# Optimization experiments

Hardware: AMD Instinct MI355X
Metric: run time of the kernel (lower is better)

## Reference

```python
import jax, jax.numpy as jnp
import numpy as np

DIM = 1024
HEADS = 16
HEAD_DIM = DIM // HEADS
EPS = 1e-6

def _layernorm(x, gamma, beta):
    # LayerNorm over last axis (head_dim), biased variance like torch
    mu = jnp.mean(x, axis=-1, keepdims=True)
    var = jnp.mean(jnp.square(x - mu), axis=-1, keepdims=True)
    return (x - mu) * jax.lax.rsqrt(var + EPS) * gamma + beta

def setup_inputs() -> dict:
    key = jax.random.key(0)
    ks = jax.random.split(key, 12)
    B, N, D = 2, 2048, DIM
    s = 1.0 / np.sqrt(D)
    inp = {
        'x': jax.random.normal(ks[0], (B, N, D), jnp.float32),
        'attn_bias': jax.random.normal(ks[1], (B, 1, N, N), jnp.float32),
        'Wq': jax.random.normal(ks[2], (D, D), jnp.float32) * s,
        'bq': jnp.zeros((D,), jnp.float32),
        'Wk': jax.random.normal(ks[3], (D, D), jnp.float32) * s,
        'bk': jnp.zeros((D,), jnp.float32),
        'Wv': jax.random.normal(ks[4], (D, D), jnp.float32) * s,
        'bv': jnp.zeros((D,), jnp.float32),
        'Wo': jax.random.normal(ks[5], (D, D), jnp.float32) * s,
        'bo': jnp.zeros((D,), jnp.float32),
        'q_gamma': jnp.ones((HEAD_DIM,), jnp.float32),
        'q_beta': jnp.zeros((HEAD_DIM,), jnp.float32),
        'k_gamma': jnp.ones((HEAD_DIM,), jnp.float32),
        'k_beta': jnp.zeros((HEAD_DIM,), jnp.float32),
    }
    return inp

def reference(x, attn_bias, Wq, bq, Wk, bk, Wv, bv, Wo, bo, q_gamma, q_beta, k_gamma, k_beta):
    B, N, D = x.shape
    h, dh = HEADS, HEAD_DIM
    # QKV projections (torch Linear: x @ W.T + b) -> (B, h, N, dh)
    def proj(W, b):
        y = jnp.einsum('bnd,ed->bne', x, W) + b
        return y.reshape(B, N, h, dh).transpose(0, 2, 1, 3)
    q = proj(Wq, bq)
    k = proj(Wk, bk)
    v = proj(Wv, bv)
    # per-head LayerNorm on Q and K
    q = _layernorm(q, q_gamma, q_beta)
    k = _layernorm(k, k_gamma, k_beta)
    # scaled dot-product attention with additive graph bias
    scores = jnp.einsum('bhnd,bhmd->bhnm', q, k) / np.sqrt(dh).astype(np.float32)
    scores = scores + attn_bias  # (B,1,N,N) broadcasts over heads
    attn = jax.nn.softmax(scores, axis=-1)
    out = jnp.einsum('bhnm,bhmd->bhnd', attn, v)
    out = out.transpose(0, 2, 1, 3).reshape(B, N, D)
    return jnp.einsum('bnd,ed->bne', out, Wo) + bo
```

## Files before the change

kernel.cpp:

```cpp
#include <hip/hip_runtime.h>
#include <hip/hip_bf16.h>
#include <hip/hip_fp16.h>

#define D_MODEL 1024
#define N_SEQ   2048
#define N_B     2
#define M_ROWS  (N_B * N_SEQ)

typedef __attribute__((ext_vector_type(8))) short bf16x8;
typedef __attribute__((ext_vector_type(4))) float f32x4;

typedef const __attribute__((address_space(1))) unsigned int gu32_t;
typedef __attribute__((address_space(3))) unsigned int lu32_t;

__device__ __forceinline__ void gload16(const void* g, void* l) {
  __builtin_amdgcn_global_load_lds((gu32_t*)g, (lu32_t*)l, 16, 0, 0);
}

__device__ inline unsigned short f2bf(float f) {
  union { float f; unsigned int u; } v; v.f = f;
  unsigned int r = (v.u + 0x7FFFu + ((v.u >> 16) & 1u)) >> 16;
  return (unsigned short)r;
}

__device__ __forceinline__ unsigned int cvt_pk_bf16(float a, float b) {
  unsigned int r;
  asm("v_cvt_pk_bf16_f32 %0, %1, %2" : "=v"(r) : "v"(a), "v"(b));
  return r;
}

__device__ __forceinline__ float exp2fast(float x) {
#if __has_builtin(__builtin_amdgcn_exp2f)
  return __builtin_amdgcn_exp2f(x);
#else
  return __expf(x * 0.69314718056f);
#endif
}

#define WAITV(N) asm volatile("s_waitcnt vmcnt(" #N ")" ::: "memory")

__device__ __forceinline__ int lds_off(int row, int col ) {
  return row * 64 + (((col >> 3) ^ (row & 7)) << 3) + (col & 7);
}

template<int ROWS, int NTHR = 256>
__device__ __forceinline__ void stage_tile(const unsigned short* gbase, size_t gstride,
                                           unsigned short* lds, int tid) {
  const int wave = tid >> 6;
#pragma unroll
  for (int rnd = 0; rnd < ROWS * 8 / NTHR; ++rnd) {
    int c = rnd * NTHR + tid;
    int row = c >> 3, pc = c & 7;
    int gcol = ((pc ^ (row & 7)) << 3);
    gload16(gbase + (size_t)row * gstride + gcol,
            lds + (size_t)(rnd * NTHR + wave * 64) * 8);
  }
}

constexpr size_t XEL = (size_t)M_ROWS * D_MODEL;
constexpr size_t WEL = (size_t)D_MODEL * D_MODEL;
constexpr size_t BEL = (size_t)N_B * N_SEQ * N_SEQ;
constexpr size_t TOTEL = XEL + 4 * WEL + BEL;

__launch_bounds__(256)
__global__ void cvt_kernel(const float* __restrict__ x, const float* __restrict__ bias,
                           const float* __restrict__ wq, const float* __restrict__ wk,
                           const float* __restrict__ wv, const float* __restrict__ wo,
                           unsigned short* __restrict__ dst,
                           unsigned short* __restrict__ dstB) {
  size_t i = ((size_t)blockIdx.x * 256 + threadIdx.x) * 8;
  if (i >= TOTEL) return;
  if (i >= XEL + 4 * WEL) {
    size_t off = i - (XEL + 4 * WEL);
    float4 f0 = *(const float4*)(bias + off);
    float4 f1 = *(const float4*)(bias + off + 4);
    __half t[8] = { __float2half(f0.x), __float2half(f0.y), __float2half(f0.z),
                    __float2half(f0.w), __float2half(f1.x), __float2half(f1.y),
                    __float2half(f1.z), __float2half(f1.w) };
    *(uint4*)(dstB + off) = *(const uint4*)t;
    return;
  }
  const float* s; size_t off = i;
  if (off < XEL)                { s = x; }
  else if (off < XEL + WEL)     { s = wq; off -= XEL; }
  else if (off < XEL + 2*WEL)   { s = wk; off -= XEL + WEL; }
  else if (off < XEL + 3*WEL)   { s = wv; off -= XEL + 2*WEL; }
  else                          { s = wo; off -= XEL + 3*WEL; }
  float4 f0 = *(const float4*)(s + off);
  float4 f1 = *(const float4*)(s + off + 4);
  unsigned short t[8] = { f2bf(f0.x), f2bf(f0.y), f2bf(f0.z), f2bf(f0.w),
                          f2bf(f1.x), f2bf(f1.y), f2bf(f1.z), f2bf(f1.w) };
  *(uint4*)(dst + i) = *(const uint4*)t;
}

__device__ __forceinline__ void mainloop128(const unsigned short* __restrict__ A,
                                            const unsigned short* __restrict__ Bw,
                                            int m0, int e0,
                                            unsigned short* As, unsigned short* Bs,
                                            f32x4 (&acc)[4][4]) {
  const int tid  = threadIdx.x;
  const int wave = tid >> 6, lane = tid & 63;
  const int l16 = lane & 15, quad = lane >> 4;
  const int wr = wave >> 1, wc = wave & 1;

  for (int kt = 0; kt < D_MODEL / 64; ++kt) {
    const int k0 = kt * 64;
    stage_tile<128>(A + (size_t)m0 * D_MODEL + k0, D_MODEL, As, tid);
    stage_tile<128>(Bw + (size_t)e0 * D_MODEL + k0, D_MODEL, Bs, tid);
    __syncthreads();
#pragma unroll
    for (int ks = 0; ks < 2; ++ks) {
      bf16x8 af[4], bfr[4];
#pragma unroll
      for (int mi = 0; mi < 4; ++mi)
        af[mi] = *(const bf16x8*)(As + lds_off(wr * 64 + mi * 16 + l16, ks * 32 + quad * 8));
#pragma unroll
      for (int ci = 0; ci < 4; ++ci)
        bfr[ci] = *(const bf16x8*)(Bs + lds_off(wc * 64 + ci * 16 + l16, ks * 32 + quad * 8));
#pragma unroll
      for (int mi = 0; mi < 4; ++mi)
#pragma unroll
        for (int ci = 0; ci < 4; ++ci)
          acc[mi][ci] = __builtin_amdgcn_mfma_f32_16x16x32_bf16(af[mi], bfr[ci], acc[mi][ci], 0, 0, 0);
    }
    __syncthreads();
  }
}

__launch_bounds__(256)
__global__ void qkv_gemm(const unsigned short* __restrict__ xb,
                         const unsigned short* __restrict__ wb,
                         const float* __restrict__ bq, const float* __restrict__ bk,
                         const float* __restrict__ bv,
                         const float* __restrict__ qg, const float* __restrict__ qbeta,
                         const float* __restrict__ kg, const float* __restrict__ kbeta,
                         unsigned short* __restrict__ qkout,
                         unsigned short* __restrict__ vt) {
  __shared__ unsigned short As[128 * 64];
  __shared__ unsigned short Bs[128 * 64];
  const int m0  = blockIdx.x * 128;
  const int by  = blockIdx.y;
  const int mat = by >> 3;
  const int e0  = (by & 7) * 128;
  const unsigned short* Bw = wb + (size_t)mat * WEL;

  f32x4 acc[4][4];
#pragma unroll
  for (int mi = 0; mi < 4; ++mi)
#pragma unroll
    for (int ci = 0; ci < 4; ++ci) acc[mi][ci] = f32x4{0.f, 0.f, 0.f, 0.f};

  mainloop128(xb, Bw, m0, e0, As, Bs, acc);

  const int lane = threadIdx.x & 63, wave = threadIdx.x >> 6;
  const int l16 = lane & 15, quad = lane >> 4;
  const int wr = wave >> 1, wc = wave & 1;
  const int colbase = e0 + wc * 64;

  const float* bias = (mat == 0) ? bq : ((mat == 1) ? bk : bv);
  float bcol[4];
#pragma unroll
  for (int ci = 0; ci < 4; ++ci) bcol[ci] = bias[colbase + ci * 16 + l16];
#pragma unroll
  for (int mi = 0; mi < 4; ++mi)
#pragma unroll
    for (int ci = 0; ci < 4; ++ci)
#pragma unroll
      for (int r = 0; r < 4; ++r) acc[mi][ci][r] += bcol[ci];

  if (mat < 2) {
    const float* gamma = (mat == 0) ? qg : kg;
    const float* beta  = (mat == 0) ? qbeta : kbeta;
    const float sc = (mat == 0) ? 0.18033688011112042f : 1.0f;
    float g4[4], bt4[4];
#pragma unroll
    for (int ci = 0; ci < 4; ++ci) {
      g4[ci] = gamma[ci * 16 + l16] * sc;
      bt4[ci] = beta[ci * 16 + l16] * sc;
    }
#pragma unroll
    for (int mi = 0; mi < 4; ++mi)
#pragma unroll
      for (int r = 0; r < 4; ++r) {
        float s = acc[mi][0][r] + acc[mi][1][r] + acc[mi][2][r] + acc[mi][3][r];
        s += __shfl_xor(s, 1); s += __shfl_xor(s, 2);
        s += __shfl_xor(s, 4); s += __shfl_xor(s, 8);
        float mean = s * (1.f / 64.f);
        float d0 = acc[mi][0][r] - mean, d1 = acc[mi][1][r] - mean;
        float d2 = acc[mi][2][r] - mean, d3 = acc[mi][3][r] - mean;
        float q = d0 * d0 + d1 * d1 + d2 * d2 + d3 * d3;
        q += __shfl_xor(q, 1); q += __shfl_xor(q, 2);
        q += __shfl_xor(q, 4); q += __shfl_xor(q, 8);
        float rs = rsqrtf(q * (1.f / 64.f) + 1e-6f);
        acc[mi][0][r] = d0 * rs * g4[0] + bt4[0];
        acc[mi][1][r] = d1 * rs * g4[1] + bt4[1];
        acc[mi][2][r] = d2 * rs * g4[2] + bt4[2];
        acc[mi][3][r] = d3 * rs * g4[3] + bt4[3];
      }
    unsigned short* out = qkout + (size_t)mat * XEL;
#pragma unroll
    for (int mi = 0; mi < 4; ++mi)
#pragma unroll
      for (int ci = 0; ci < 4; ++ci) {
        int col = colbase + ci * 16 + l16;
#pragma unroll
        for (int r = 0; r < 4; ++r) {
          int row = m0 + wr * 64 + mi * 16 + quad * 4 + r;
          out[(size_t)row * D_MODEL + col] = f2bf(acc[mi][ci][r]);
        }
      }
  } else {
    unsigned short* scr = ((wave < 2) ? As : Bs) + (size_t)(wave & 1) * 4096;
#pragma unroll
    for (int ci = 0; ci < 4; ++ci) {
      int dl = ci * 16 + l16;
      int sw = (dl & 3) * 16;
#pragma unroll
      for (int mi = 0; mi < 4; ++mi)
#pragma unroll
        for (int r = 0; r < 4; ++r) {
          int np = ((mi >> 1) << 5) + (quad << 3) + ((mi & 1) << 2) + r;
          scr[dl * 64 + (np ^ sw)] = f2bf(acc[mi][ci][r]);
        }
    }
    __builtin_amdgcn_wave_barrier();
    int row0 = m0 + wr * 64;
    int b = row0 >> 11, nb = row0 & 2047;
    int h = colbase >> 6;
    int dl = lane;
    unsigned short* gdst = vt + ((size_t)((b * 16 + h) * 64 + dl) * N_SEQ + nb);
    const unsigned short* srow = scr + dl * 64;
    int sw = (dl & 3) * 16;
#pragma unroll
    for (int j = 0; j < 8; ++j) {
      uint4 vv = *(const uint4*)(srow + ((j * 8) ^ sw));
      *(uint4*)(gdst + j * 8) = vv;
    }
  }
}

__launch_bounds__(256)
__global__ void out_gemm(const unsigned short* __restrict__ ao,
                         const unsigned short* __restrict__ wob,
                         const float* __restrict__ bo,
                         float* __restrict__ out) {
  __shared__ unsigned short As[128 * 64];
  __shared__ unsigned short Bs[128 * 64];
  const int m0 = blockIdx.x * 128;
  const int e0 = blockIdx.y * 128;

  f32x4 acc[4][4];
#pragma unroll
  for (int mi = 0; mi < 4; ++mi)
#pragma unroll
    for (int ci = 0; ci < 4; ++ci) acc[mi][ci] = f32x4{0.f, 0.f, 0.f, 0.f};

  mainloop128(ao, wob, m0, e0, As, Bs, acc);

  const int lane = threadIdx.x & 63, wave = threadIdx.x >> 6;
  const int l16 = lane & 15, quad = lane >> 4;
  const int wr = wave >> 1, wc = wave & 1;
  float bcol[4];
#pragma unroll
  for (int ci = 0; ci < 4; ++ci) bcol[ci] = bo[e0 + wc * 64 + ci * 16 + l16];
#pragma unroll
  for (int mi = 0; mi < 4; ++mi)
#pragma unroll
    for (int ci = 0; ci < 4; ++ci) {
      int col = e0 + wc * 64 + ci * 16 + l16;
#pragma unroll
      for (int r = 0; r < 4; ++r) {
        int row = m0 + wr * 64 + mi * 16 + quad * 4 + r;
        out[(size_t)row * D_MODEL + col] = acc[mi][ci][r] + bcol[ci];
      }
    }
}

__launch_bounds__(512)
__global__ void attn_kernel(const unsigned short* __restrict__ Q,
                            const unsigned short* __restrict__ Kn,
                            const unsigned short* __restrict__ Vt,
                            const unsigned short* __restrict__ bias16,
                            unsigned short* __restrict__ Out) {
  __shared__ unsigned short smem[24576];

  const int tid  = threadIdx.x;
  const int wave = tid >> 6, lane = tid & 63;
  const int quad = lane >> 4, l16 = lane & 15;
  const int pairId = wave >> 1;
  const int kh = wave & 1;
  const int bidx = blockIdx.x;
  const int qt = bidx & 15;
  const int h  = (bidx >> 4) & 15;
  const int b  = bidx >> 8;
  const int q0 = qt * 128;
  const size_t base  = (size_t)b * N_SEQ * D_MODEL + (size_t)h * 64;
  const unsigned short* vtb = Vt + (size_t)(b * 16 + h) * 64 * N_SEQ;

  const unsigned short* brow[2];
#pragma unroll
  for (int mi = 0; mi < 2; ++mi)
    brow[mi] = bias16 + ((size_t)b * N_SEQ + q0 + pairId * 32 + mi * 16 + l16) * N_SEQ;
  const int bcol0 = kh * 32 + quad * 4;

  stage_tile<128, 512>(Q + base + (size_t)q0 * D_MODEL, D_MODEL, smem, tid);
  __syncthreads();

  bf16x8 aq[2][2];
#pragma unroll
  for (int mi = 0; mi < 2; ++mi)
#pragma unroll
    for (int ks = 0; ks < 2; ++ks)
      aq[mi][ks] = *(const bf16x8*)(smem + lds_off(pairId * 32 + mi * 16 + l16, ks * 32 + quad * 8));
  __syncthreads();

  uint2 bcur[2][2];
#pragma unroll
  for (int mi = 0; mi < 2; ++mi)
#pragma unroll
    for (int cl = 0; cl < 2; ++cl)
      bcur[mi][cl] = *(const uint2*)(brow[mi] + bcol0 + cl * 16);

  stage_tile<64, 512>(Kn + base, D_MODEL, smem, tid);
  stage_tile<64, 512>(vtb, N_SEQ, smem + 12288, tid);
  stage_tile<64, 512>(Kn + base + (size_t)64 * D_MODEL, D_MODEL, smem + 4096, tid);
  stage_tile<64, 512>(vtb + 64, N_SEQ, smem + 12288 + 4096, tid);

  WAITV(2);
  __builtin_amdgcn_s_barrier();
  __builtin_amdgcn_sched_barrier(0);

  f32x4 o[2][4];
#pragma unroll
  for (int mi = 0; mi < 2; ++mi)
#pragma unroll
    for (int cd = 0; cd < 4; ++cd) o[mi][cd] = f32x4{0.f, 0.f, 0.f, 0.f};
  float lsum[2] = {0.f, 0.f};
  constexpr float LOG2E = 1.44269504088896340736f;

  constexpr int NT = N_SEQ / 64;
  for (int kt = 0; kt < NT; ++kt) {
    const int cur = kt % 3;
    unsigned short* Kcur = smem + cur * 4096;
    unsigned short* Vcur = smem + 12288 + cur * 4096;

    if (kt + 2 < NT) {
      const int nb = (kt + 2) % 3;
      stage_tile<64, 512>(Kn + base + (size_t)(kt + 2) * 64 * D_MODEL, D_MODEL,
                          smem + nb * 4096, tid);
      stage_tile<64, 512>(vtb + (kt + 2) * 64, N_SEQ,
                          smem + 12288 + nb * 4096, tid);
    }

    f32x4 sfT[2][2];
#pragma unroll
    for (int cl = 0; cl < 2; ++cl) {
      const int c = kh * 2 + cl;
      bf16x8 k0 = *(const bf16x8*)(Kcur + lds_off(c * 16 + l16, quad * 8));
      bf16x8 k1 = *(const bf16x8*)(Kcur + lds_off(c * 16 + l16, 32 + quad * 8));
      __builtin_amdgcn_s_setprio(1);
#pragma unroll
      for (int mi = 0; mi < 2; ++mi) {
        f32x4 z = f32x4{0.f, 0.f, 0.f, 0.f};
        z = __builtin_amdgcn_mfma_f32_16x16x32_bf16(k0, aq[mi][0], z, 0, 0, 0);
        sfT[mi][cl] = __builtin_amdgcn_mfma_f32_16x16x32_bf16(k1, aq[mi][1], z, 0, 0, 0);
      }
      __builtin_amdgcn_s_setprio(0);
    }

    union PafU { unsigned int w[4]; bf16x8 v; };
    PafU paf[2];
#pragma unroll
    for (int mi = 0; mi < 2; ++mi)
#pragma unroll
      for (int cl = 0; cl < 2; ++cl) {
        uint2 bw = bcur[mi][cl];
        float2 fa = __half22float2(*(const __half2*)&bw.x);
        float2 fb = __half22float2(*(const __half2*)&bw.y);
        float p0 = exp2fast(fmaf(fa.x, LOG2E, sfT[mi][cl][0]));
        float p1 = exp2fast(fmaf(fa.y, LOG2E, sfT[mi][cl][1]));
        float p2 = exp2fast(fmaf(fb.x, LOG2E, sfT[mi][cl][2]));
        float p3 = exp2fast(fmaf(fb.y, LOG2E, sfT[mi][cl][3]));
        lsum[mi] += (p0 + p1) + (p2 + p3);
        paf[mi].w[cl * 2]     = cvt_pk_bf16(p0, p1);
        paf[mi].w[cl * 2 + 1] = cvt_pk_bf16(p2, p3);
      }

    if (kt + 1 < NT) {
#pragma unroll
      for (int mi = 0; mi < 2; ++mi)
#pragma unroll
        for (int cl = 0; cl < 2; ++cl)
          bcur[mi][cl] = *(const uint2*)(brow[mi] + (kt + 1) * 64 + bcol0 + cl * 16);
    }

    {
      bf16x8 bv[4];
#pragma unroll
      for (int cd = 0; cd < 4; ++cd)
        bv[cd] = *(const bf16x8*)(Vcur + lds_off(cd * 16 + l16, kh * 32 + quad * 8));
      __builtin_amdgcn_s_setprio(1);
#pragma unroll
      for (int mi = 0; mi < 2; ++mi)
#pragma unroll
        for (int cd = 0; cd < 4; ++cd)
          o[mi][cd] = __builtin_amdgcn_mfma_f32_16x16x32_bf16(bv[cd], paf[mi].v, o[mi][cd], 0, 0, 0);
      __builtin_amdgcn_s_setprio(0);
    }

    if (kt + 1 < NT) {
      if (kt < NT - 2) { WAITV(6); } else { WAITV(4); }
      __builtin_amdgcn_s_barrier();
      __builtin_amdgcn_sched_barrier(0);
    }
  }

  WAITV(0);
  __syncthreads();

  float* red = (float*)smem;
  float* slot = red + (size_t)(pairId * 64 + lane) * 34;
  if (kh) {
#pragma unroll
    for (int mi = 0; mi < 2; ++mi)
#pragma unroll
      for (int cd = 0; cd < 4; ++cd)
#pragma unroll
        for (int r = 0; r < 4; ++r)
          slot[mi * 16 + cd * 4 + r] = o[mi][cd][r];
    slot[32] = lsum[0];
    slot[33] = lsum[1];
  }
  __syncthreads();
  if (!kh) {
#pragma unroll
    for (int mi = 0; mi < 2; ++mi)
#pragma unroll
      for (int cd = 0; cd < 4; ++cd)
#pragma unroll
        for (int r = 0; r < 4; ++r)
          o[mi][cd][r] += slot[mi * 16 + cd * 4 + r];
    lsum[0] += slot[32];
    lsum[1] += slot[33];

#pragma unroll
    for (int mi = 0; mi < 2; ++mi) {
      float l = lsum[mi];
      l += __shfl_xor(l, 16);
      l += __shfl_xor(l, 32);
      float inv = 1.0f / l;
      size_t row = (size_t)b * N_SEQ + q0 + pairId * 32 + mi * 16 + l16;
#pragma unroll
      for (int cd = 0; cd < 4; ++cd) {
        uint2 vv;
        vv.x = cvt_pk_bf16(o[mi][cd][0] * inv, o[mi][cd][1] * inv);
        vv.y = cvt_pk_bf16(o[mi][cd][2] * inv, o[mi][cd][3] * inv);
        *(uint2*)(Out + row * D_MODEL + h * 64 + cd * 16 + quad * 4) = vv;
      }
    }
  }
}

extern "C" void kernel_launch(void* const* d_in, const int* in_sizes, int n_in,
                              void* d_out, int out_size, void* d_ws, size_t ws_size,
                              hipStream_t stream) {
  const float* x    = (const float*)d_in[0];
  const float* bias = (const float*)d_in[1];
  const float* Wq = (const float*)d_in[2];  const float* bq = (const float*)d_in[3];
  const float* Wk = (const float*)d_in[4];  const float* bk = (const float*)d_in[5];
  const float* Wv = (const float*)d_in[6];  const float* bv = (const float*)d_in[7];
  const float* Wo = (const float*)d_in[8];  const float* bo = (const float*)d_in[9];
  const float* qg = (const float*)d_in[10]; const float* qb = (const float*)d_in[11];
  const float* kg = (const float*)d_in[12]; const float* kb = (const float*)d_in[13];
  float* out = (float*)d_out;

  unsigned short* wsb = (unsigned short*)d_ws;
  unsigned short* xb  = wsb;
  unsigned short* wqb = wsb + XEL;
  unsigned short* wob = wsb + XEL + 3 * WEL;
  unsigned short* qn  = wsb + XEL + 4 * WEL;
  unsigned short* kn  = qn + XEL;
  unsigned short* vt  = qn + 2 * XEL;
  unsigned short* b16 = qn + 3 * XEL;
  unsigned short* ao  = xb;

  dim3 blk(256, 1, 1);

  cvt_kernel<<<dim3((unsigned)(TOTEL / (256 * 8)), 1, 1), blk, 0, stream>>>(
      x, bias, Wq, Wk, Wv, Wo, wsb, b16);

  qkv_gemm<<<dim3(M_ROWS / 128, 24, 1), blk, 0, stream>>>(
      xb, wqb, bq, bk, bv, qg, qb, kg, kb, qn, vt);

  attn_kernel<<<dim3(N_B * 16 * (N_SEQ / 128), 1, 1), dim3(512, 1, 1), 0, stream>>>(
      qn, kn, vt, b16, ao);

  out_gemm<<<dim3(M_ROWS / 128, D_MODEL / 128, 1), blk, 0, stream>>>(ao, wob, bo, out);
}
```

Measured before the change: 262.4 us.

## Stage attention bias tiles through LDS with double-buffered K/V/bias pipeline

Moves the per-thread direct global loads of the fp16 attention bias into the async global-to-LDS staging pipeline, loading a 128x64 bias tile alongside each K and V tile. The ring changes from a three-deep K/V buffer to a two-deep buffer covering K, V and bias, and LDS grows to 64 KB. Launch bounds now request 4 blocks per CU. The aim is coalesced bias loads that overlap with compute, at the cost of a shallower prefetch distance and more LDS per block, which may limit occupancy.

```diff
diff --git a/kernel.cpp b/kernel.cpp
--- a/kernel.cpp
+++ b/kernel.cpp
@@ -276,13 +276,13 @@
     }
 }
 
-__launch_bounds__(512)
+__launch_bounds__(512, 4)
 __global__ void attn_kernel(const unsigned short* __restrict__ Q,
                             const unsigned short* __restrict__ Kn,
                             const unsigned short* __restrict__ Vt,
                             const unsigned short* __restrict__ bias16,
                             unsigned short* __restrict__ Out) {
-  __shared__ unsigned short smem[24576];
+  __shared__ unsigned short smem[32768];
 
   const int tid  = threadIdx.x;
   const int wave = tid >> 6, lane = tid & 63;
@@ -296,11 +296,7 @@
   const int q0 = qt * 128;
   const size_t base  = (size_t)b * N_SEQ * D_MODEL + (size_t)h * 64;
   const unsigned short* vtb = Vt + (size_t)(b * 16 + h) * 64 * N_SEQ;
-
-  const unsigned short* brow[2];
-#pragma unroll
-  for (int mi = 0; mi < 2; ++mi)
-    brow[mi] = bias16 + ((size_t)b * N_SEQ + q0 + pairId * 32 + mi * 16 + l16) * N_SEQ;
+  const unsigned short* bbase = bias16 + ((size_t)b * N_SEQ + q0) * N_SEQ;
   const int bcol0 = kh * 32 + quad * 4;
 
   stage_tile<128, 512>(Q + base + (size_t)q0 * D_MODEL, D_MODEL, smem, tid);
@@ -314,19 +310,11 @@
       aq[mi][ks] = *(const bf16x8*)(smem + lds_off(pairId * 32 + mi * 16 + l16, ks * 32 + quad * 8));
   __syncthreads();
 
-  uint2 bcur[2][2];
-#pragma unroll
-  for (int mi = 0; mi < 2; ++mi)
-#pragma unroll
-    for (int cl = 0; cl < 2; ++cl)
-      bcur[mi][cl] = *(const uint2*)(brow[mi] + bcol0 + cl * 16);
-
   stage_tile<64, 512>(Kn + base, D_MODEL, smem, tid);
-  stage_tile<64, 512>(vtb, N_SEQ, smem + 12288, tid);
-  stage_tile<64, 512>(Kn + base + (size_t)64 * D_MODEL, D_MODEL, smem + 4096, tid);
-  stage_tile<64, 512>(vtb + 64, N_SEQ, smem + 12288 + 4096, tid);
-
-  WAITV(2);
+  stage_tile<64, 512>(vtb, N_SEQ, smem + 8192, tid);
+  stage_tile<128, 512>(bbase, N_SEQ, smem + 16384, tid);
+
+  WAITV(0);
   __builtin_amdgcn_s_barrier();
   __builtin_amdgcn_sched_barrier(0);
 
@@ -340,17 +328,31 @@
 
   constexpr int NT = N_SEQ / 64;
   for (int kt = 0; kt < NT; ++kt) {
-    const int cur = kt % 3;
+    const int cur = kt & 1;
     unsigned short* Kcur = smem + cur * 4096;
-    unsigned short* Vcur = smem + 12288 + cur * 4096;
-
-    if (kt + 2 < NT) {
-      const int nb = (kt + 2) % 3;
-      stage_tile<64, 512>(Kn + base + (size_t)(kt + 2) * 64 * D_MODEL, D_MODEL,
+    unsigned short* Vcur = smem + 8192 + cur * 4096;
+    const unsigned short* Bcur = smem + 16384 + cur * 8192;
+
+    if (kt + 1 < NT) {
+      const int nb = cur ^ 1;
+      stage_tile<64, 512>(Kn + base + (size_t)(kt + 1) * 64 * D_MODEL, D_MODEL,
                           smem + nb * 4096, tid);
-      stage_tile<64, 512>(vtb + (kt + 2) * 64, N_SEQ,
-                          smem + 12288 + nb * 4096, tid);
-    }
+      stage_tile<64, 512>(vtb + (kt + 1) * 64, N_SEQ,
+                          smem + 8192 + nb * 4096, tid);
+      stage_tile<128, 512>(bbase + (kt + 1) * 64, N_SEQ,
+                           smem + 16384 + nb * 8192, tid);
+      WAITV(4);
+    } else {
+      WAITV(0);
+    }
+
+    uint2 breg[2][2];
+#pragma unroll
+    for (int mi = 0; mi < 2; ++mi)
+#pragma unroll
+      for (int cl = 0; cl < 2; ++cl)
+        breg[mi][cl] = *(const uint2*)(Bcur +
+            lds_off(pairId * 32 + mi * 16 + l16, bcol0 + cl * 16));
 
     f32x4 sfT[2][2];
 #pragma unroll
@@ -374,7 +376,7 @@
     for (int mi = 0; mi < 2; ++mi)
 #pragma unroll
       for (int cl = 0; cl < 2; ++cl) {
-        uint2 bw = bcur[mi][cl];
+        uint2 bw = breg[mi][cl];
         float2 fa = __half22float2(*(const __half2*)&bw.x);
         float2 fb = __half22float2(*(const __half2*)&bw.y);
         float p0 = exp2fast(fmaf(fa.x, LOG2E, sfT[mi][cl][0]));
@@ -386,14 +388,6 @@
         paf[mi].w[cl * 2 + 1] = cvt_pk_bf16(p2, p3);
       }
 
-    if (kt + 1 < NT) {
-#pragma unroll
-      for (int mi = 0; mi < 2; ++mi)
-#pragma unroll
-        for (int cl = 0; cl < 2; ++cl)
-          bcur[mi][cl] = *(const uint2*)(brow[mi] + (kt + 1) * 64 + bcol0 + cl * 16);
-    }
-
     {
       bf16x8 bv[4];
 #pragma unroll
@@ -409,7 +403,7 @@
     }
 
     if (kt + 1 < NT) {
-      if (kt < NT - 2) { WAITV(6); } else { WAITV(4); }
+      WAITV(2);
       __builtin_amdgcn_s_barrier();
       __builtin_amdgcn_sched_barrier(0);
     }
```

After: 235.8 us. -10.1%, faster.
